# Kernel optimization log

Hardware: AMD Instinct MI355X
Metric: run time of the kernel (lower is better)

## Reference

```python
import jax, jax.numpy as jnp
import numpy as np

EMBED_DIM = 2048
NUM_HEADS = 16
HEAD_DIM = EMBED_DIM // NUM_HEADS
BATCH, SEQ = 4, 4096


def setup_inputs() -> dict:
    key = jax.random.key(0)
    k1, k2, k3, k4 = jax.random.split(key, 4)
    scale = 1.0 / np.sqrt(EMBED_DIM)
    x = jax.random.normal(k1, (BATCH, SEQ, EMBED_DIM), dtype=jnp.float32)
    W_qkv = jax.random.normal(k2, (EMBED_DIM, 3 * EMBED_DIM), dtype=jnp.float32) * scale
    W_out = jax.random.normal(k3, (EMBED_DIM, EMBED_DIM), dtype=jnp.float32) * scale
    b_out = jax.random.normal(k4, (EMBED_DIM,), dtype=jnp.float32) * 0.01
    return {"x": x, "W_qkv": W_qkv, "W_out": W_out, "b_out": b_out}


def reference(x, W_qkv, W_out, b_out):
    b, s, _ = x.shape
    # qkv: (b, s, 3, h, d)
    qkv = (x @ W_qkv).reshape(b, s, 3, NUM_HEADS, HEAD_DIM)
    q, k, v = qkv[:, :, 0], qkv[:, :, 1], qkv[:, :, 2]
    # NOTE: faithful to source — scores mix HEADS per token: (b, s, h, h)
    scores = jnp.einsum('bshd,bsHd->bshH', q, k) / jnp.sqrt(jnp.float32(HEAD_DIM))
    w = jax.nn.softmax(scores, axis=-1)
    attn = jnp.einsum('bshH,bsHd->bshd', w, v).reshape(b, s, EMBED_DIM)
    return attn @ W_out + b_out
```

## Files before the change

### kernel.cpp

```cpp
#include <hip/hip_runtime.h>
#include <hip/hip_bf16.h>
#include <cstdint>


#define TOKENS 16384
#define EMB    2048
#define NQKV   6144

typedef __bf16 bf16x8_t __attribute__((ext_vector_type(8)));
typedef float  f32x4_t  __attribute__((ext_vector_type(4)));

#define GLOAD16(gsrc, ldst)                                                    \
  __builtin_amdgcn_global_load_lds(                                            \
      (const __attribute__((address_space(1))) void*)(uintptr_t)(gsrc),        \
      (__attribute__((address_space(3))) void*)(uint32_t)(uintptr_t)(ldst),    \
      16, 0, 0)

static __device__ __forceinline__ unsigned short f32_to_bf16_bits(float f) {
  union { float f; uint32_t u; } x; x.f = f;
  uint32_t u = x.u;
  u += 0x7fffu + ((u >> 16) & 1u);
  return (unsigned short)(u >> 16);
}

__global__ __launch_bounds__(256) void cvt_f32_bf16(
    const float4* __restrict__ in, ushort4* __restrict__ out, int n4) {
  const int stride = gridDim.x * blockDim.x;
  for (int i = blockIdx.x * blockDim.x + threadIdx.x; i < n4; i += stride) {
    float4 v = in[i];
    ushort4 o;
    o.x = f32_to_bf16_bits(v.x);
    o.y = f32_to_bf16_bits(v.y);
    o.z = f32_to_bf16_bits(v.z);
    o.w = f32_to_bf16_bits(v.w);
    out[i] = o;
  }
}

__global__ __launch_bounds__(256) void transpose_cvt(
    const float* __restrict__ in, unsigned short* __restrict__ out, int R, int C) {
  __shared__ float tile[32][33];
  const int bx = blockIdx.x * 32;
  const int by = blockIdx.y * 32;
  const int tx = threadIdx.x;
  const int ty = threadIdx.y;
#pragma unroll
  for (int j = 0; j < 32; j += 8)
    tile[ty + j][tx] = in[(size_t)(by + ty + j) * C + bx + tx];
  __syncthreads();
#pragma unroll
  for (int j = 0; j < 32; j += 8)
    out[(size_t)(bx + ty + j) * R + by + tx] = f32_to_bf16_bits(tile[tx][ty + j]);
}

template <bool OUT_BF16>
__global__ __launch_bounds__(512, 1) void gemm_bt(
    const unsigned short* __restrict__ A,
    const unsigned short* __restrict__ BT,
    unsigned short* __restrict__ Cb,
    float* __restrict__ Cf,
    const float* __restrict__ bias,
    int M, int N) {
  constexpr int K = 2048;
  constexpr int BK = 64;
  constexpr int NKT = K / BK;
  __shared__ __align__(16) char lds[131072];

  const int nbx = N / 256;
  const int nwg = gridDim.x;
  const int bid = blockIdx.x;
  const int swzb = (bid & 7) * (nwg >> 3) + (bid >> 3);
  const int by = swzb / nbx;
  const int bx = swzb % nbx;

  const int t    = threadIdx.x;
  const int lane = t & 63;
  const int wid  = t >> 6;
  const int wr   = wid >> 2;
  const int wc   = wid & 3;
  const int lr   = lane & 15;
  const int g    = lane >> 4;

  const unsigned short* aSrc = A  + (size_t)by * 256 * K;
  const unsigned short* bSrc = BT + (size_t)bx * 256 * K;

  int aoff[2], boff[2];
#pragma unroll
  for (int i = 0; i < 2; ++i) {
    const int p   = (i * 512 + t) * 16;
    const int lo  = p ^ (((p >> 7) & 7) << 4);
    const int rih = lo >> 7;
    const int kbe = (lo & 127) >> 1;
    aoff[i] = (((rih >> 6) << 7) + (rih & 63)) * K + kbe;
    boff[i] = (((rih >> 5) << 6) + (rih & 31)) * K + kbe;
  }
  const int ldst = wid << 10;

  auto stageA = [&](int h, int k0, char* bufA) {
#pragma unroll
    for (int i = 0; i < 2; ++i)
      GLOAD16(aSrc + aoff[i] + h * (64 * K) + k0, bufA + h * 16384 + i * 8192 + ldst);
  };
  auto stageB = [&](int h, int k0, char* bufB) {
#pragma unroll
    for (int i = 0; i < 2; ++i)
      GLOAD16(bSrc + boff[i] + h * (32 * K) + k0, bufB + h * 16384 + i * 8192 + ldst);
  };

  const int sw   = (lr & 7) << 4;
  const int col0 = (g * 16) ^ sw;
  const int col1 = (64 + g * 16) ^ sw;
  const int aRow = (wr * 64 + lr) * 128;
  const int bRow = (wc * 32 + lr) * 128;

  f32x4_t acc[8][4] = {};
  bf16x8_t av[4][2];
  bf16x8_t bv[4][2];

#define LDA(bufA, q)                                                           \
  {                                                                            \
    const char* _b = (bufA) + (q) * 16384 + aRow;                              \
    _Pragma("unroll") for (int m2 = 0; m2 < 4; ++m2) {                         \
      av[m2][0] = *(const bf16x8_t*)(_b + m2 * 2048 + col0);                   \
      av[m2][1] = *(const bf16x8_t*)(_b + m2 * 2048 + col1);                   \
    }                                                                          \
  }
#define LDB(bufB, pair)                                                        \
  {                                                                            \
    _Pragma("unroll") for (int e = 0; e < 2; ++e) {                            \
      const int nf = (pair) * 2 + e;                                           \
      const char* _b = (bufB) + (nf >> 1) * 16384 + (nf & 1) * 2048 + bRow;    \
      bv[nf][0] = *(const bf16x8_t*)(_b + col0);                               \
      bv[nf][1] = *(const bf16x8_t*)(_b + col1);                               \
    }                                                                          \
  }
#define MFMA16(q, pair)                                                        \
  _Pragma("unroll") for (int m2 = 0; m2 < 4; ++m2)                             \
  _Pragma("unroll") for (int e = 0; e < 2; ++e)                                \
  _Pragma("unroll") for (int ks = 0; ks < 2; ++ks)                             \
    acc[(q) * 4 + m2][(pair) * 2 + e] = __builtin_amdgcn_mfma_f32_16x16x32_bf16( \
        av[m2][ks], bv[(pair) * 2 + e][ks], acc[(q) * 4 + m2][(pair) * 2 + e], 0, 0, 0);

#define PHASE_TAIL                                                             \
  __builtin_amdgcn_s_barrier();                                                \
  asm volatile("s_waitcnt lgkmcnt(0)" ::: "memory");                           \
  __builtin_amdgcn_sched_barrier(0);

#define PHASE_END                                                              \
  __builtin_amdgcn_s_setprio(0);                                               \
  __builtin_amdgcn_sched_barrier(0);                                           \
  __builtin_amdgcn_s_barrier();

  {
    char* b0 = lds;
    char* b0B = lds + 32768;
    char* b1 = lds + 65536;
    char* b1B = b1 + 32768;
    stageA(0, 0, b0);
    stageB(1, 0, b0B);
    stageA(1, 0, b0);
    stageB(0, 0, b0B);
    stageA(0, BK, b1);
    stageB(1, BK, b1B);
    asm volatile("s_waitcnt vmcnt(4)" ::: "memory");
    __builtin_amdgcn_s_barrier();
  }

  for (int kt = 0; kt < NKT; ++kt) {
    char* cA = lds + (kt & 1) * 65536;
    char* cB = cA + 32768;
    char* nA = lds + ((kt + 1) & 1) * 65536;
    char* nB = nA + 32768;
    const int k1 = (kt + 1) * BK;
    const int k2 = (kt + 2) * BK;
    const bool s1 = (kt + 1) < NKT;
    const bool s2 = (kt + 2) < NKT;

    LDA(cA, 0);
    LDB(cB, 0);
    if (s1) stageA(1, k1, nA);
    PHASE_TAIL
    __builtin_amdgcn_s_setprio(1);
    MFMA16(0, 0);
    PHASE_END

    LDB(cB, 1);
    if (s1) stageB(0, k1, nB);
    PHASE_TAIL
    __builtin_amdgcn_s_setprio(1);
    MFMA16(0, 1);
    PHASE_END

    LDA(cA, 1);
    if (s2) stageA(0, k2, cA);
    PHASE_TAIL
    __builtin_amdgcn_s_setprio(1);
    MFMA16(1, 1);
    PHASE_END

    if (s2) stageB(1, k2, cB);
    if (s2) { asm volatile("s_waitcnt vmcnt(4)" ::: "memory"); }
    else    { asm volatile("s_waitcnt vmcnt(0)" ::: "memory"); }
    PHASE_TAIL
    __builtin_amdgcn_s_setprio(1);
    MFMA16(1, 0);
    PHASE_END
  }

  const int rbase = by * 256 + wr * 128 + g * 4;
  const int cbase = bx * 256 + wc * 64 + lr;
#pragma unroll
  for (int m = 0; m < 8; ++m) {
#pragma unroll
    for (int nf = 0; nf < 4; ++nf) {
      const int col = cbase + nf * 16;
#pragma unroll
      for (int j = 0; j < 4; ++j) {
        const size_t off = (size_t)(rbase + (m >> 2) * 64 + (m & 3) * 16 + j) * N + col;
        if constexpr (OUT_BF16) {
          Cb[off] = f32_to_bf16_bits(acc[m][nf][j]);
        } else {
          Cf[off] = acc[m][nf][j] + bias[col];
        }
      }
    }
  }
#undef LDA
#undef LDB
#undef MFMA16
#undef PHASE_TAIL
#undef PHASE_END
}

__global__ __launch_bounds__(256) void attn_heads(
    const unsigned short* __restrict__ qkv,
    unsigned short* __restrict__ attn) {
  __shared__ __align__(16) unsigned short sQKV[NQKV];
  __shared__ float sW[16][16];

  const int t = threadIdx.x;
  const size_t qbase = (size_t)blockIdx.x * NQKV;

  const uint4* gp = (const uint4*)(qkv + qbase);
  uint4* l = (uint4*)sQKV;
#pragma unroll
  for (int i = 0; i < 3; ++i) {
    const int idx = i * 256 + t;
    int dst = idx;
    if (idx >= 256 && idx < 512) {
      const int r = (idx - 256) >> 4;
      const int c = idx & 15;
      dst = 256 + r * 16 + (c ^ (r & 7));
    }
    l[dst] = gp[idx];
  }
  __syncthreads();

  const int h = t >> 4;
  const int H = t & 15;
  const bf16x8_t* q8 = (const bf16x8_t*)sQKV + h * 16;
  const bf16x8_t* k8 = (const bf16x8_t*)sQKV + 256;
  float s = 0.f;
#pragma unroll
  for (int d8 = 0; d8 < 16; ++d8) {
    bf16x8_t qv = q8[d8];
    bf16x8_t kv = k8[H * 16 + (d8 ^ (H & 7))];
#pragma unroll
    for (int j = 0; j < 8; ++j)
      s = fmaf((float)qv[j], (float)kv[j], s);
  }
  s *= 0.08838834764831843f;

  float mx = s;
#pragma unroll
  for (int o = 8; o; o >>= 1) mx = fmaxf(mx, __shfl_xor(mx, o));
  const float e = __expf(s - mx);
  float sum = e;
#pragma unroll
  for (int o = 8; o; o >>= 1) sum += __shfl_xor(sum, o);
  sW[h][H] = e / sum;
  __syncthreads();

  const int d0c = t & 15;
  const bf16x8_t* v8 = (const bf16x8_t*)sQKV + 512;
  float accv[8] = {};
#pragma unroll
  for (int j = 0; j < 16; ++j) {
    const float w = sW[h][j];
    const bf16x8_t vv = v8[j * 16 + d0c];
#pragma unroll
    for (int jj = 0; jj < 8; ++jj)
      accv[jj] = fmaf(w, (float)vv[jj], accv[jj]);
  }
  bf16x8_t o;
#pragma unroll
  for (int jj = 0; jj < 8; ++jj) o[jj] = (__bf16)accv[jj];
  *(bf16x8_t*)(attn + (size_t)blockIdx.x * EMB + h * 128 + d0c * 8) = o;
}

extern "C" void kernel_launch(void* const* d_in, const int* in_sizes, int n_in,
                              void* d_out, int out_size, void* d_ws, size_t ws_size,
                              hipStream_t stream) {
  const float* x    = (const float*)d_in[0];
  const float* Wqkv = (const float*)d_in[1];
  const float* Wout = (const float*)d_in[2];
  const float* bout = (const float*)d_in[3];
  float* out = (float*)d_out;

  unsigned short* xb    = (unsigned short*)d_ws;
  unsigned short* wqkvT = xb    + (size_t)33554432;
  unsigned short* woutT = wqkvT + (size_t)12582912;
  unsigned short* qkv   = woutT + (size_t)4194304;
  unsigned short* attn  = qkv   + (size_t)100663296;

  cvt_f32_bf16<<<2048, 256, 0, stream>>>((const float4*)x, (ushort4*)xb, 33554432 / 4);
  transpose_cvt<<<dim3(6144 / 32, 2048 / 32), dim3(32, 8), 0, stream>>>(Wqkv, wqkvT, 2048, 6144);
  transpose_cvt<<<dim3(2048 / 32, 2048 / 32), dim3(32, 8), 0, stream>>>(Wout, woutT, 2048, 2048);
  gemm_bt<true><<<(16384 / 256) * (6144 / 256), 512, 0, stream>>>(
      xb, wqkvT, qkv, nullptr, nullptr, 16384, 6144);
  attn_heads<<<TOKENS, 256, 0, stream>>>(qkv, attn);
  gemm_bt<false><<<(16384 / 256) * (2048 / 256), 512, 0, stream>>>(
      attn, woutT, nullptr, out, bout, 16384, 2048);
}
```

Before: 621.4 us.

## Software-pipeline LDS fragment loads across GEMM phases with double register buffers

Restructures the bf16 GEMM main loop so the A and B register fragments for the next k-tile are loaded from LDS during the current tile's last phases. It uses two register sets for A and ping-pong B fragments, and unrolls the k-loop by two. The per-phase lgkmcnt(0) wait is removed so LDS reads can overlap MFMAs. The global-to-LDS staging order and the vmcnt thresholds are reshuffled to match. This raises register pressure and assumes NKT is even.

```diff
diff --git a/kernel.cpp b/kernel.cpp
--- a/kernel.cpp
+++ b/kernel.cpp
@@ -114,97 +114,88 @@
   const int bRow = (wc * 32 + lr) * 128;
 
   f32x4_t acc[8][4] = {};
-  bf16x8_t av[4][2];
-  bf16x8_t bv[4][2];
-
-#define LDA(bufA, q)                                                           \
+  bf16x8_t av0[4][2], av1[4][2];
+  bf16x8_t bv1[2][2];
+  bf16x8_t bv0A[2][2], bv0B[2][2];
+
+#define LDA_INTO(dst, bufA_, q)                                                \
   {                                                                            \
-    const char* _b = (bufA) + (q) * 16384 + aRow;                              \
+    const char* _b = (bufA_) + (q) * 16384 + aRow;                             \
     _Pragma("unroll") for (int m2 = 0; m2 < 4; ++m2) {                         \
-      av[m2][0] = *(const bf16x8_t*)(_b + m2 * 2048 + col0);                   \
-      av[m2][1] = *(const bf16x8_t*)(_b + m2 * 2048 + col1);                   \
+      dst[m2][0] = *(const bf16x8_t*)(_b + m2 * 2048 + col0);                  \
+      dst[m2][1] = *(const bf16x8_t*)(_b + m2 * 2048 + col1);                  \
     }                                                                          \
   }
-#define LDB(bufB, pair)                                                        \
+#define LDB_INTO(dst, bufB_, pair)                                             \
   {                                                                            \
     _Pragma("unroll") for (int e = 0; e < 2; ++e) {                            \
       const int nf = (pair) * 2 + e;                                           \
-      const char* _b = (bufB) + (nf >> 1) * 16384 + (nf & 1) * 2048 + bRow;    \
-      bv[nf][0] = *(const bf16x8_t*)(_b + col0);                               \
-      bv[nf][1] = *(const bf16x8_t*)(_b + col1);                               \
+      const char* _b = (bufB_) + (nf >> 1) * 16384 + (nf & 1) * 2048 + bRow;   \
+      dst[e][0] = *(const bf16x8_t*)(_b + col0);                               \
+      dst[e][1] = *(const bf16x8_t*)(_b + col1);                               \
     }                                                                          \
   }
-#define MFMA16(q, pair)                                                        \
+#define MFMAQ(AV, BV, Q, PAIR)                                                 \
   _Pragma("unroll") for (int m2 = 0; m2 < 4; ++m2)                             \
   _Pragma("unroll") for (int e = 0; e < 2; ++e)                                \
   _Pragma("unroll") for (int ks = 0; ks < 2; ++ks)                             \
-    acc[(q) * 4 + m2][(pair) * 2 + e] = __builtin_amdgcn_mfma_f32_16x16x32_bf16( \
-        av[m2][ks], bv[(pair) * 2 + e][ks], acc[(q) * 4 + m2][(pair) * 2 + e], 0, 0, 0);
-
-#define PHASE_TAIL                                                             \
-  __builtin_amdgcn_s_barrier();                                                \
-  asm volatile("s_waitcnt lgkmcnt(0)" ::: "memory");                           \
-  __builtin_amdgcn_sched_barrier(0);
-
+    acc[(Q) * 4 + m2][(PAIR) * 2 + e] = __builtin_amdgcn_mfma_f32_16x16x32_bf16( \
+        AV[m2][ks], BV[e][ks], acc[(Q) * 4 + m2][(PAIR) * 2 + e], 0, 0, 0);
+
+#define SBR __builtin_amdgcn_sched_barrier(0)
+#define PHASE_MID                                                              \
+  SBR; __builtin_amdgcn_s_barrier(); SBR; __builtin_amdgcn_s_setprio(1);
 #define PHASE_END                                                              \
-  __builtin_amdgcn_s_setprio(0);                                               \
-  __builtin_amdgcn_sched_barrier(0);                                           \
-  __builtin_amdgcn_s_barrier();
+  __builtin_amdgcn_s_setprio(0); SBR; __builtin_amdgcn_s_barrier();
+
+#define SUBITER(KT, BVC, BVN, CU)                                              \
+  {                                                                            \
+    char* curA = lds + (CU) * 65536;                                           \
+    char* curB = curA + 32768;                                                 \
+    char* nxtA = lds + ((CU) ^ 1) * 65536;                                     \
+    char* nxtB = nxtA + 32768;                                                 \
+    const int k2  = ((KT) + 2) * BK;                                           \
+    const bool s1 = (KT) + 1 < NKT;                                            \
+    const bool s2 = (KT) + 2 < NKT;                                            \
+                                         \
+    LDB_INTO(bv1, curB, 1);                                                    \
+    PHASE_MID; MFMAQ(av0, BVC, 0, 0); PHASE_END;                               \
+                   \
+    LDA_INTO(av1, curA, 1);                                                    \
+    if (s2) { stageB(0, k2, curB); stageB(1, k2, curB); }                      \
+    PHASE_MID; MFMAQ(av0, bv1, 0, 1); PHASE_END;                               \
+            \
+    if (s1) {                                                                  \
+      if (s2) { asm volatile("s_waitcnt vmcnt(4)" ::: "memory"); }             \
+      else    { asm volatile("s_waitcnt vmcnt(0)" ::: "memory"); }             \
+      LDA_INTO(av0, nxtA, 0);                                                  \
+    }                                                                          \
+    if (s2) stageA(0, k2, curA);                                               \
+    PHASE_MID; MFMAQ(av1, bv1, 1, 1); PHASE_END;                               \
+            \
+    if (s1) LDB_INTO(BVN, nxtB, 0);                                            \
+    if (s2) stageA(1, k2, curA);                                               \
+    PHASE_MID; MFMAQ(av1, BVC, 1, 0); PHASE_END;                               \
+  }
 
   {
-    char* b0 = lds;
+    char* b0A = lds;
     char* b0B = lds + 32768;
-    char* b1 = lds + 65536;
-    char* b1B = b1 + 32768;
-    stageA(0, 0, b0);
-    stageB(1, 0, b0B);
-    stageA(1, 0, b0);
-    stageB(0, 0, b0B);
-    stageA(0, BK, b1);
-    stageB(1, BK, b1B);
-    asm volatile("s_waitcnt vmcnt(4)" ::: "memory");
+    char* b1A = lds + 65536;
+    char* b1B = b1A + 32768;
+    stageA(0, 0, b0A); stageA(1, 0, b0A);
+    stageB(0, 0, b0B); stageB(1, 0, b0B);
+    stageA(0, BK, b1A); stageA(1, BK, b1A);
+    stageB(0, BK, b1B); stageB(1, BK, b1B);
+    asm volatile("s_waitcnt vmcnt(8)" ::: "memory");
     __builtin_amdgcn_s_barrier();
-  }
-
-  for (int kt = 0; kt < NKT; ++kt) {
-    char* cA = lds + (kt & 1) * 65536;
-    char* cB = cA + 32768;
-    char* nA = lds + ((kt + 1) & 1) * 65536;
-    char* nB = nA + 32768;
-    const int k1 = (kt + 1) * BK;
-    const int k2 = (kt + 2) * BK;
-    const bool s1 = (kt + 1) < NKT;
-    const bool s2 = (kt + 2) < NKT;
-
-    LDA(cA, 0);
-    LDB(cB, 0);
-    if (s1) stageA(1, k1, nA);
-    PHASE_TAIL
-    __builtin_amdgcn_s_setprio(1);
-    MFMA16(0, 0);
-    PHASE_END
-
-    LDB(cB, 1);
-    if (s1) stageB(0, k1, nB);
-    PHASE_TAIL
-    __builtin_amdgcn_s_setprio(1);
-    MFMA16(0, 1);
-    PHASE_END
-
-    LDA(cA, 1);
-    if (s2) stageA(0, k2, cA);
-    PHASE_TAIL
-    __builtin_amdgcn_s_setprio(1);
-    MFMA16(1, 1);
-    PHASE_END
-
-    if (s2) stageB(1, k2, cB);
-    if (s2) { asm volatile("s_waitcnt vmcnt(4)" ::: "memory"); }
-    else    { asm volatile("s_waitcnt vmcnt(0)" ::: "memory"); }
-    PHASE_TAIL
-    __builtin_amdgcn_s_setprio(1);
-    MFMA16(1, 0);
-    PHASE_END
+    LDA_INTO(av0, b0A, 0);
+    LDB_INTO(bv0A, b0B, 0);
+  }
+
+  for (int kt = 0; kt < NKT; kt += 2) {
+    SUBITER(kt,     bv0A, bv0B, 0);
+    SUBITER(kt + 1, bv0B, bv0A, 1);
   }
 
   const int rbase = by * 256 + wr * 128 + g * 4;
@@ -225,11 +216,13 @@
       }
     }
   }
-#undef LDA
-#undef LDB
-#undef MFMA16
-#undef PHASE_TAIL
+#undef LDA_INTO
+#undef LDB_INTO
+#undef MFMAQ
+#undef SBR
+#undef PHASE_MID
 #undef PHASE_END
+#undef SUBITER
 }
 
 __global__ __launch_bounds__(256) void attn_heads(
```

New measurement: 1.534 ms. 147% more time.
